# Performance work log

Measured on AMD Instinct MI355X. Metric: run time of the kernel, lower is better.

## Reference

```python
import jax, jax.numpy as jnp
import numpy as np

NEG_INIT = -1.0e9  # matches torch.full(..., -1000000000.0)

def setup_inputs() -> dict:
    key = jax.random.key(0)
    ks = jax.random.split(key, 12)
    N, B, F, C = 4_000_000, 16384, 3, 4
    flat_muons = jax.random.normal(ks[0], (N, F), dtype=jnp.float32)
    batch_index = jnp.sort(jax.random.randint(ks[1], (N,), 0, B))
    conditions = jax.random.normal(ks[2], (B, C), dtype=jnp.float32)
    def lin(k, fin, fout):
        k1, k2 = jax.random.split(k)
        bound = 1.0 / np.sqrt(fin)
        W = jax.random.uniform(k1, (fin, fout), jnp.float32, -bound, bound)
        b = jax.random.uniform(k2, (fout,), jnp.float32, -bound, bound)
        return W, b
    W1, b1 = lin(ks[3], F + C, 64)
    W2, b2 = lin(ks[4], 64, 128)
    W3, b3 = lin(ks[5], 128 + C, 128)
    W4, b4 = lin(ks[6], 128, 1)
    return {"flat_muons": flat_muons, "batch_index": batch_index,
            "conditions": conditions, "batch_size": B,
            "W1": W1, "b1": b1, "W2": W2, "b2": b2,
            "W3": W3, "b3": b3, "W4": W4, "b4": b4}

def reference(flat_muons, batch_index, conditions, batch_size,
              W1, b1, W2, b2, W3, b3, W4, b4):
    lrelu = lambda x: jax.nn.leaky_relu(x, 0.2)
    flat_cond = conditions[batch_index]                       # [N, C] gather
    point_in = jnp.concatenate([flat_muons, flat_cond], axis=1)
    h = lrelu(point_in @ W1 + b1)                             # [N, 64]
    point_feats = lrelu(h @ W2 + b2)                          # [N, 128]
    # segmented amax with -1e9 baseline (scatter_reduce_ amax semantics)
    global_feats = jnp.full((batch_size, 128), NEG_INIT, dtype=point_feats.dtype)
    global_feats = global_feats.at[batch_index].max(point_feats)
    decision_in = jnp.concatenate([global_feats, conditions], axis=1)
    score = lrelu(decision_in @ W3 + b3) @ W4 + b4            # [B, 1]
    return score
```

## Files before the change

kernel.cpp:

```cpp
#include <hip/hip_runtime.h>

typedef float f32x4 __attribute__((ext_vector_type(4)));
typedef float f32x16 __attribute__((ext_vector_type(16)));
typedef _Float16 half8 __attribute__((ext_vector_type(8)));
typedef _Float16 half2v __attribute__((ext_vector_type(2)));
typedef unsigned u32x4 __attribute__((ext_vector_type(4)));

__device__ __forceinline__ unsigned f2mono(float f) {
  unsigned u = __float_as_uint(f);
  return (u & 0x80000000u) ? ~u : (u | 0x80000000u);
}
__device__ __forceinline__ float mono2f(unsigned u) {
  return (u & 0x80000000u) ? __uint_as_float(u & 0x7fffffffu) : __uint_as_float(~u);
}
__device__ __forceinline__ float lrelu(float x) { return fmaxf(x, 0.2f * x); }
__device__ __forceinline__ unsigned pkrtz(float a, float b) {
  return __builtin_bit_cast(unsigned, __builtin_amdgcn_cvt_pkrtz(a, b));
}
__device__ __forceinline__ unsigned lrelu_pk(float a, float b) {
  const half2v v = __builtin_bit_cast(half2v, pkrtz(a, b));
  const half2v s = v * (half2v){(_Float16)0.2f, (_Float16)0.2f};
  return __builtin_bit_cast(unsigned, __builtin_elementwise_max(v, s));
}
__device__ __forceinline__ half8 ash8(u32x4 u) { return __builtin_bit_cast(half8, u); }
__device__ __forceinline__ float max16(const f32x16& a) {
  const float m1 = fmaxf(fmaxf(a[0], a[1]), a[2]);
  const float m2 = fmaxf(fmaxf(a[3], a[4]), a[5]);
  const float m3 = fmaxf(fmaxf(a[6], a[7]), a[8]);
  const float m4 = fmaxf(fmaxf(a[9], a[10]), a[11]);
  const float m5 = fmaxf(fmaxf(a[12], a[13]), a[14]);
  return fmaxf(fmaxf(fmaxf(m1, m2), m3), fmaxf(fmaxf(m4, m5), a[15]));
}
__device__ __forceinline__ void plswap(unsigned& x, unsigned& y) {
  asm volatile("v_permlane32_swap_b32 %0, %1" : "+v"(x), "+v"(y));
}
__device__ __forceinline__ float xhalf_max(float m) {
  unsigned a = __float_as_uint(m), b = a;
  plswap(a, b);
  return fmaxf(__uint_as_float(a), __uint_as_float(b));
}

__global__ void sc_init(unsigned* __restrict__ gf, int total4) {
  int i = blockIdx.x * blockDim.x + threadIdx.x;
  if (i < total4) {
    unsigned m = f2mono(-1.0e9f);
    ((uint4*)gf)[i] = make_uint4(m, m, m, m);
  }
}

__global__ __launch_bounds__(256, 2) void sc_main(
    const float* __restrict__ muons, const int* __restrict__ bidx,
    const float* __restrict__ cond, const float* __restrict__ W1,
    const float* __restrict__ b1, const float* __restrict__ W2,
    const float* __restrict__ b2, unsigned* __restrict__ gf, int N, int CPW) {
  __shared__ __align__(16) _Float16 w2f[8192];
  __shared__ __align__(16) _Float16 w1e[1024];

  const int t = threadIdx.x;
  const int w = t >> 6;
  const int lane = t & 63;
  const int col = lane & 31;
  const int kh2 = lane >> 5;

  {
    const int j = t & 127, kh = t >> 7;
    for (int kk = 0; kk < 32; ++kk) {
      const int k = kh * 32 + kk;
      w2f[((k >> 3) * 128 + j) * 8 + (k & 7)] = (_Float16)W2[k * 128 + j];
    }
  }
  if (t < 128) {
    const int j = t & 63, kc = t >> 6;
    for (int e = 0; e < 8; ++e) {
      const int kp = kc * 8 + e;
      float val;
      if (kp < 7)       val = W1[kp * 64 + j];
      else if (kp < 14) val = W1[(kp - 7) * 64 + j];
      else if (kp == 14) val = b1[j];
      else { const float b = b1[j]; val = b - (float)(_Float16)b; }
      w1e[(kc * 64 + j) * 8 + e] = (_Float16)val;
    }
  }
  __syncthreads();

  float b2v[4];
  #pragma unroll
  for (int jt = 0; jt < 4; ++jt) b2v[jt] = b2[jt * 32 + col];
  f32x16 zf;
  #pragma unroll
  for (int e = 0; e < 16; ++e) zf[e] = 0.0f;

  const int gwave = blockIdx.x * 4 + w;
  const int start = gwave * CPW;
  if (start >= N) return;
  const int end = min(start + CPW, N);
  const int prevb = (start == 0) ? -1 : bidx[start - 1];
  const int nextb = (end >= N) ? -1 : bidx[end];
  int run_b = bidx[start];
  float run_s[4];
  #pragma unroll
  for (int jt = 0; jt < 4; ++jt) run_s[jt] = -3.0e38f;

  const half8 a1lo = *(const half8*)&w1e[(kh2 * 64 + col) * 8];
  const half8 a1hi = *(const half8*)&w1e[(kh2 * 64 + 32 + col) * 8];

  auto FLUSH = [&](int b, const float* m) {
    const bool interior = (b != prevb) && (b != nextb);
    float mm[4];
    #pragma unroll
    for (int jt = 0; jt < 4; ++jt) mm[jt] = xhalf_max(m[jt]);
    if (lane < 32) {
      #pragma unroll
      for (int jt = 0; jt < 4; ++jt) {
        if (mm[jt] > -2.9e38f) {
          const unsigned enc = f2mono(lrelu(mm[jt] + b2v[jt]));
          unsigned* addr = &gf[b * 128 + jt * 32 + col];
          if (interior) *addr = enc; else atomicMax(addr, enc);
        }
      }
    }
  };

  auto DECOMP = [&](float mu0, float mu1, float mu2, const f32x4& c4) -> half8 {
    float in[7];
    in[0] = mu0; in[1] = mu1; in[2] = mu2;
    in[3] = c4.x; in[4] = c4.y; in[5] = c4.z; in[6] = c4.w;
    const unsigned pA0 = pkrtz(in[0], in[1]);
    const unsigned pA1 = pkrtz(in[2], in[3]);
    const unsigned pA2 = pkrtz(in[4], in[5]);
    const half2v hA0 = __builtin_bit_cast(half2v, pA0);
    const half2v hA1 = __builtin_bit_cast(half2v, pA1);
    const half2v hA2 = __builtin_bit_cast(half2v, pA2);
    const float xl0 = in[0] - (float)hA0[0];
    const unsigned pA3 = pkrtz(in[6], xl0);
    const half2v hA3 = __builtin_bit_cast(half2v, pA3);
    const unsigned pB0 = pkrtz(in[1] - (float)hA0[1], in[2] - (float)hA1[0]);
    const unsigned pB1 = pkrtz(in[3] - (float)hA1[1], in[4] - (float)hA2[0]);
    const unsigned pB2 = pkrtz(in[5] - (float)hA2[1], in[6] - (float)hA3[0]);
    const unsigned pB3 = 0x3C003C00u;
    u32x4 bu;
    bu[0] = kh2 ? pB0 : pA0;
    bu[1] = kh2 ? pB1 : pA1;
    bu[2] = kh2 ? pB2 : pA2;
    bu[3] = kh2 ? pB3 : pA3;
    return ash8(bu);
  };

  auto MKAFRAG = [&](const f32x16& a0, const f32x16& a1, half8* Afr) {
    unsigned pk0[8], pk1[8];
    #pragma unroll
    for (int q = 0; q < 4; ++q) {
      pk0[2 * q]     = lrelu_pk(a0[4 * q],     a0[4 * q + 1]);
      pk0[2 * q + 1] = lrelu_pk(a0[4 * q + 2], a0[4 * q + 3]);
      pk1[2 * q]     = lrelu_pk(a1[4 * q],     a1[4 * q + 1]);
      pk1[2 * q + 1] = lrelu_pk(a1[4 * q + 2], a1[4 * q + 3]);
    }
    #pragma unroll
    for (int ks = 0; ks < 4; ++ks) {
      const unsigned* s = (ks < 2) ? pk0 : pk1;
      const int base = (ks & 1) * 4;
      unsigned x0 = s[base + 0], y0 = s[base + 2];
      unsigned x1 = s[base + 1], y1 = s[base + 3];
      plswap(x0, y0);
      plswap(x1, y1);
      u32x4 au;
      au[0] = x0; au[1] = x1; au[2] = y0; au[3] = y1;
      Afr[ks] = ash8(au);
    }
  };

  auto L2SEG = [&](const half8* Afr, int bi) {
    f32x16 acc2[4];
    #pragma unroll
    for (int ks = 0; ks < 4; ++ks) {
      const int kcb = (2 * ks + kh2) * 128;
      #pragma unroll
      for (int jt = 0; jt < 4; ++jt) {
        const half8 B = *(const half8*)&w2f[(kcb + jt * 32 + col) * 8];
        acc2[jt] = __builtin_amdgcn_mfma_f32_32x32x16_f16(Afr[ks], B,
                                                          (ks == 0) ? zf : acc2[jt], 0, 0, 0);
      }
    }
    const int bA = __shfl(bi, 0);
    const int bB = __shfl(bi, 31);
    if (bA != run_b) {
      FLUSH(run_b, run_s);
      #pragma unroll
      for (int jt = 0; jt < 4; ++jt) run_s[jt] = -3.0e38f;
      run_b = bA;
    }
    if (bA == bB) {
      #pragma unroll
      for (int jt = 0; jt < 4; ++jt)
        run_s[jt] = fmaxf(run_s[jt], max16(acc2[jt]));
    } else {
      const unsigned long long ball = __ballot(bi == bA);
      const int split = (int)__popcll(ball & 0xffffffffULL);
      const int bS = __shfl(bi, split);
      if (bS == bB) {
        float mA[4], mB[4];
        #pragma unroll
        for (int jt = 0; jt < 4; ++jt) { mA[jt] = -3.0e38f; mB[jt] = -3.0e38f; }
        #pragma unroll
        for (int r = 0; r < 16; ++r) {
          const int rr = (r & 3) + ((r >> 2) << 3) + (kh2 << 2);
          const bool inA = rr < split;
          #pragma unroll
          for (int jt = 0; jt < 4; ++jt) {
            const float v = acc2[jt][r];
            mA[jt] = fmaxf(mA[jt], inA ? v : -3.0e38f);
            mB[jt] = fmaxf(mB[jt], inA ? -3.0e38f : v);
          }
        }
        #pragma unroll
        for (int jt = 0; jt < 4; ++jt) mA[jt] = fmaxf(mA[jt], run_s[jt]);
        FLUSH(bA, mA);
        #pragma unroll
        for (int jt = 0; jt < 4; ++jt) run_s[jt] = mB[jt];
        run_b = bB;
      } else {
        int pbi[16];
        #pragma unroll
        for (int r = 0; r < 16; ++r) {
          const int rr = (r & 3) + ((r >> 2) << 3) + (kh2 << 2);
          pbi[r] = __shfl(bi, rr);
        }
        for (int b = bA; b <= bB; ++b) {
          float m[4];
          #pragma unroll
          for (int jt = 0; jt < 4; ++jt) {
            float mm = -3.0e38f;
            #pragma unroll
            for (int r = 0; r < 16; ++r)
              if (pbi[r] == b) mm = fmaxf(mm, acc2[jt][r]);
            if (b == bA) mm = fmaxf(mm, run_s[jt]);
            m[jt] = mm;
          }
          if (b < bB) {
            FLUSH(b, m);
          } else {
            #pragma unroll
            for (int jt = 0; jt < 4; ++jt) run_s[jt] = m[jt];
          }
        }
        run_b = bB;
      }
    }
  };

  int pA = min(start + col, N - 1);
  int pB = min(start + 32 + col, N - 1);
  int biA_n = bidx[pA], biB_n = bidx[pB];
  float muA_n[3] = {muons[pA * 3], muons[pA * 3 + 1], muons[pA * 3 + 2]};
  float muB_n[3] = {muons[pB * 3], muons[pB * 3 + 1], muons[pB * 3 + 2]};
  f32x4 c4A_n = *(const f32x4*)&cond[biA_n * 4];
  f32x4 c4B_n = *(const f32x4*)&cond[biB_n * 4];

  for (int pbase = start; pbase < end; pbase += 64) {
    const int biA = biA_n, biB = biB_n;
    const float mA0 = muA_n[0], mA1 = muA_n[1], mA2 = muA_n[2];
    const float mB0 = muB_n[0], mB1 = muB_n[1], mB2 = muB_n[2];
    const f32x4 c4A = c4A_n, c4B = c4B_n;

    const int pnA = min(pbase + 64 + col, N - 1);
    const int pnB = min(pbase + 96 + col, N - 1);
    biA_n = bidx[pnA]; biB_n = bidx[pnB];
    muA_n[0] = muons[pnA * 3]; muA_n[1] = muons[pnA * 3 + 1]; muA_n[2] = muons[pnA * 3 + 2];
    muB_n[0] = muons[pnB * 3]; muB_n[1] = muons[pnB * 3 + 1]; muB_n[2] = muons[pnB * 3 + 2];

    const half8 bfrA = DECOMP(mA0, mA1, mA2, c4A);
    const half8 bfrB = DECOMP(mB0, mB1, mB2, c4B);
    const f32x16 aA0 = __builtin_amdgcn_mfma_f32_32x32x16_f16(a1lo, bfrA, zf, 0, 0, 0);
    const f32x16 aA1 = __builtin_amdgcn_mfma_f32_32x32x16_f16(a1hi, bfrA, zf, 0, 0, 0);
    const f32x16 aB0 = __builtin_amdgcn_mfma_f32_32x32x16_f16(a1lo, bfrB, zf, 0, 0, 0);
    const f32x16 aB1 = __builtin_amdgcn_mfma_f32_32x32x16_f16(a1hi, bfrB, zf, 0, 0, 0);

    c4A_n = *(const f32x4*)&cond[biA_n * 4];
    c4B_n = *(const f32x4*)&cond[biB_n * 4];

    half8 AfrA[4], AfrB[4];
    MKAFRAG(aA0, aA1, AfrA);
    MKAFRAG(aB0, aB1, AfrB);

    L2SEG(AfrA, biA);
    L2SEG(AfrB, biB);
  }
  FLUSH(run_b, run_s);
}

__global__ __launch_bounds__(256, 2) void sc_final(
    const unsigned* __restrict__ gf, const float* __restrict__ cond,
    const float* __restrict__ W3, const float* __restrict__ b3,
    const float* __restrict__ W4, const float* __restrict__ b4,
    float* __restrict__ out, int B) {
  __shared__ __align__(16) _Float16 w3h[18432];
  __shared__ __align__(16) _Float16 w3l[18432];
  __shared__ float w4s[128];
  const int t = threadIdx.x;
  const int w = t >> 6, lane = t & 63, col = lane & 31, kh2 = lane >> 5;

  for (int i = t; i < 144 * 128; i += 256) {
    const int k = i >> 7, j = i & 127;
    float v = 0.0f;
    if (k < 132) v = W3[k * 128 + j];
    else if (k == 132) v = b3[j];
    const _Float16 h = (_Float16)v;
    const int a = ((k >> 3) * 128 + j) * 8 + (k & 7);
    w3h[a] = h;
    w3l[a] = (_Float16)(v - (float)h);
  }
  if (t < 128) w4s[t] = W4[t];
  __syncthreads();

  const int tile = blockIdx.x * 4 + w;
  const int row = tile * 32 + col;
  const int rc = min(row, B - 1);

  uint4 g[16];
  #pragma unroll
  for (int kc = 0; kc < 8; ++kc) {
    const int base = rc * 128 + kc * 16 + kh2 * 8;
    g[2 * kc]     = *(const uint4*)&gf[base];
    g[2 * kc + 1] = *(const uint4*)&gf[base + 4];
  }
  const f32x4 c4 = *(const f32x4*)&cond[rc * 4];

  f32x16 zf;
  #pragma unroll
  for (int e = 0; e < 16; ++e) zf[e] = 0.0f;
  f32x16 acc[4];

  #pragma unroll
  for (int kc = 0; kc < 9; ++kc) {
    float v[8];
    if (kc < 8) {
      const uint4 ga = g[2 * kc], gb = g[2 * kc + 1];
      v[0] = mono2f(ga.x); v[1] = mono2f(ga.y); v[2] = mono2f(ga.z); v[3] = mono2f(ga.w);
      v[4] = mono2f(gb.x); v[5] = mono2f(gb.y); v[6] = mono2f(gb.z); v[7] = mono2f(gb.w);
    } else if (kh2 == 0) {
      v[0] = c4.x; v[1] = c4.y; v[2] = c4.z; v[3] = c4.w;
      v[4] = 1.0f; v[5] = 0.0f; v[6] = 0.0f; v[7] = 0.0f;
    } else {
      #pragma unroll
      for (int e = 0; e < 8; ++e) v[e] = 0.0f;
    }
    u32x4 bh, bl;
    #pragma unroll
    for (int q = 0; q < 4; ++q) {
      const unsigned ph = pkrtz(v[2 * q], v[2 * q + 1]);
      const half2v hh = __builtin_bit_cast(half2v, ph);
      bh[q] = ph;
      bl[q] = pkrtz(v[2 * q] - (float)hh[0], v[2 * q + 1] - (float)hh[1]);
    }
    const half8 Bh = ash8(bh), Bl = ash8(bl);
    #pragma unroll
    for (int jt = 0; jt < 4; ++jt) {
      const int a = ((kc * 2 + kh2) * 128 + jt * 32 + col) * 8;
      const half8 Ah = *(const half8*)&w3h[a];
      const half8 Al = *(const half8*)&w3l[a];
      f32x16 c = (kc == 0) ? zf : acc[jt];
      c = __builtin_amdgcn_mfma_f32_32x32x16_f16(Ah, Bh, c, 0, 0, 0);
      c = __builtin_amdgcn_mfma_f32_32x32x16_f16(Ah, Bl, c, 0, 0, 0);
      c = __builtin_amdgcn_mfma_f32_32x32x16_f16(Al, Bh, c, 0, 0, 0);
      acc[jt] = c;
    }
  }

  float partial = 0.0f;
  #pragma unroll
  for (int jt = 0; jt < 4; ++jt)
    #pragma unroll
    for (int r = 0; r < 16; ++r) {
      const int j = jt * 32 + (r & 3) + ((r >> 2) << 3) + (kh2 << 2);
      partial += lrelu(acc[jt][r]) * w4s[j];
    }
  unsigned pa = __float_as_uint(partial), pb = pa;
  plswap(pa, pb);
  const float tot = __uint_as_float(pa) + __uint_as_float(pb);
  if (lane < 32 && row < B) out[row] = tot + b4[0];
}

extern "C" void kernel_launch(void* const* d_in, const int* in_sizes, int n_in,
                              void* d_out, int out_size, void* d_ws, size_t ws_size,
                              hipStream_t stream) {
  const float* muons = (const float*)d_in[0];
  const int* bidx = (const int*)d_in[1];
  const float* cond = (const float*)d_in[2];
  const float* W1 = (const float*)d_in[4];
  const float* b1 = (const float*)d_in[5];
  const float* W2 = (const float*)d_in[6];
  const float* b2 = (const float*)d_in[7];
  const float* W3 = (const float*)d_in[8];
  const float* b3 = (const float*)d_in[9];
  const float* W4 = (const float*)d_in[10];
  const float* b4 = (const float*)d_in[11];
  float* out = (float*)d_out;
  const int N = in_sizes[1];
  const int B = out_size;
  unsigned* gf = (unsigned*)d_ws;

  const int total4 = (B * 128) / 4;
  sc_init<<<(total4 + 255) / 256, 256, 0, stream>>>(gf, total4);

  const int nblocks = 2048;
  const int nwaves = nblocks * 4;
  const int cpw = (((N + nwaves - 1) / nwaves) + 63) & ~63;
  sc_main<<<nblocks, 256, 0, stream>>>(muons, bidx, cond, W1, b1, W2, b2, gf, N, cpw);

  const int ftiles = (B + 31) / 32;
  const int fblocks = (ftiles + 3) / 4;
  sc_final<<<fblocks, 256, 0, stream>>>(gf, cond, W3, b3, W4, b4, out, B);
  (void)n_in; (void)ws_size;
}
```

Measured before the change: 124.2 us.

## Split layer-2 MFMA accumulators into halves and raise occupancy to three blocks

The layer-2 MFMA loop now computes two 32-column tiles at a time instead of all four, and the segmented max reduction and flush run per half. This cuts the number of live f32x16 accumulators from four to two, lowering register pressure. Launch bounds for sc_main go from 2 to 3 blocks per CU to use the freed registers for occupancy. The cost is that boundary-handling logic (ballot, split and shuffles) and the flush path run twice per segment, and there is less MFMA ILP within a wave.

```diff
diff --git a/kernel.cpp b/kernel.cpp
--- a/kernel.cpp
+++ b/kernel.cpp
@@ -48,7 +48,7 @@
   }
 }
 
-__global__ __launch_bounds__(256, 2) void sc_main(
+__global__ __launch_bounds__(256, 3) void sc_main(
     const float* __restrict__ muons, const int* __restrict__ bidx,
     const float* __restrict__ cond, const float* __restrict__ W1,
     const float* __restrict__ b1, const float* __restrict__ W2,
@@ -104,19 +104,20 @@
   const half8 a1lo = *(const half8*)&w1e[(kh2 * 64 + col) * 8];
   const half8 a1hi = *(const half8*)&w1e[(kh2 * 64 + 32 + col) * 8];
 
-  auto FLUSH = [&](int b, const float* m) {
+  auto FLUSH2 = [&](int b, int jtb, float m0, float m1) {
     const bool interior = (b != prevb) && (b != nextb);
-    float mm[4];
-    #pragma unroll
-    for (int jt = 0; jt < 4; ++jt) mm[jt] = xhalf_max(m[jt]);
+    const float g0 = xhalf_max(m0);
+    const float g1 = xhalf_max(m1);
     if (lane < 32) {
-      #pragma unroll
-      for (int jt = 0; jt < 4; ++jt) {
-        if (mm[jt] > -2.9e38f) {
-          const unsigned enc = f2mono(lrelu(mm[jt] + b2v[jt]));
-          unsigned* addr = &gf[b * 128 + jt * 32 + col];
-          if (interior) *addr = enc; else atomicMax(addr, enc);
-        }
+      if (g0 > -2.9e38f) {
+        const unsigned enc = f2mono(lrelu(g0 + b2v[jtb]));
+        unsigned* addr = &gf[b * 128 + jtb * 32 + col];
+        if (interior) *addr = enc; else atomicMax(addr, enc);
+      }
+      if (g1 > -2.9e38f) {
+        const unsigned enc = f2mono(lrelu(g1 + b2v[jtb + 1]));
+        unsigned* addr = &gf[b * 128 + (jtb + 1) * 32 + col];
+        if (interior) *addr = enc; else atomicMax(addr, enc);
       }
     }
   };
@@ -170,54 +171,54 @@
   };
 
   auto L2SEG = [&](const half8* Afr, int bi) {
-    f32x16 acc2[4];
-    #pragma unroll
-    for (int ks = 0; ks < 4; ++ks) {
-      const int kcb = (2 * ks + kh2) * 128;
-      #pragma unroll
-      for (int jt = 0; jt < 4; ++jt) {
-        const half8 B = *(const half8*)&w2f[(kcb + jt * 32 + col) * 8];
-        acc2[jt] = __builtin_amdgcn_mfma_f32_32x32x16_f16(Afr[ks], B,
-                                                          (ks == 0) ? zf : acc2[jt], 0, 0, 0);
-      }
-    }
     const int bA = __shfl(bi, 0);
     const int bB = __shfl(bi, 31);
     if (bA != run_b) {
-      FLUSH(run_b, run_s);
+      FLUSH2(run_b, 0, run_s[0], run_s[1]);
+      FLUSH2(run_b, 2, run_s[2], run_s[3]);
       #pragma unroll
       for (int jt = 0; jt < 4; ++jt) run_s[jt] = -3.0e38f;
       run_b = bA;
     }
-    if (bA == bB) {
+    const bool fast = (bA == bB);
+    int split = 0, bS = 0;
+    if (!fast) {
+      const unsigned long long ball = __ballot(bi == bA);
+      split = (int)__popcll(ball & 0xffffffffULL);
+      bS = __shfl(bi, split);
+    }
+
+    #pragma unroll
+    for (int jh = 0; jh < 2; ++jh) {
+      const int jt0 = jh * 2, jt1 = jh * 2 + 1;
+      f32x16 a0, a1;
       #pragma unroll
-      for (int jt = 0; jt < 4; ++jt)
-        run_s[jt] = fmaxf(run_s[jt], max16(acc2[jt]));
-    } else {
-      const unsigned long long ball = __ballot(bi == bA);
-      const int split = (int)__popcll(ball & 0xffffffffULL);
-      const int bS = __shfl(bi, split);
-      if (bS == bB) {
-        float mA[4], mB[4];
-        #pragma unroll
-        for (int jt = 0; jt < 4; ++jt) { mA[jt] = -3.0e38f; mB[jt] = -3.0e38f; }
+      for (int ks = 0; ks < 4; ++ks) {
+        const int kcb = (2 * ks + kh2) * 128;
+        const half8 B0 = *(const half8*)&w2f[(kcb + jt0 * 32 + col) * 8];
+        const half8 B1 = *(const half8*)&w2f[(kcb + jt1 * 32 + col) * 8];
+        a0 = __builtin_amdgcn_mfma_f32_32x32x16_f16(Afr[ks], B0, (ks == 0) ? zf : a0, 0, 0, 0);
+        a1 = __builtin_amdgcn_mfma_f32_32x32x16_f16(Afr[ks], B1, (ks == 0) ? zf : a1, 0, 0, 0);
+      }
+
+      if (fast) {
+        run_s[jt0] = fmaxf(run_s[jt0], max16(a0));
+        run_s[jt1] = fmaxf(run_s[jt1], max16(a1));
+      } else if (bS == bB) {
+        float mA0 = -3.0e38f, mA1 = -3.0e38f, mB0 = -3.0e38f, mB1 = -3.0e38f;
         #pragma unroll
         for (int r = 0; r < 16; ++r) {
           const int rr = (r & 3) + ((r >> 2) << 3) + (kh2 << 2);
           const bool inA = rr < split;
-          #pragma unroll
-          for (int jt = 0; jt < 4; ++jt) {
-            const float v = acc2[jt][r];
-            mA[jt] = fmaxf(mA[jt], inA ? v : -3.0e38f);
-            mB[jt] = fmaxf(mB[jt], inA ? -3.0e38f : v);
-          }
+          const float v0 = a0[r], v1 = a1[r];
+          mA0 = fmaxf(mA0, inA ? v0 : -3.0e38f);
+          mA1 = fmaxf(mA1, inA ? v1 : -3.0e38f);
+          mB0 = fmaxf(mB0, inA ? -3.0e38f : v0);
+          mB1 = fmaxf(mB1, inA ? -3.0e38f : v1);
         }
-        #pragma unroll
-        for (int jt = 0; jt < 4; ++jt) mA[jt] = fmaxf(mA[jt], run_s[jt]);
-        FLUSH(bA, mA);
-        #pragma unroll
-        for (int jt = 0; jt < 4; ++jt) run_s[jt] = mB[jt];
-        run_b = bB;
+        FLUSH2(bA, jt0, fmaxf(mA0, run_s[jt0]), fmaxf(mA1, run_s[jt1]));
+        run_s[jt0] = mB0;
+        run_s[jt1] = mB1;
       } else {
         int pbi[16];
         #pragma unroll
@@ -226,26 +227,21 @@
           pbi[r] = __shfl(bi, rr);
         }
         for (int b = bA; b <= bB; ++b) {
-          float m[4];
+          float m0 = -3.0e38f, m1 = -3.0e38f;
           #pragma unroll
-          for (int jt = 0; jt < 4; ++jt) {
-            float mm = -3.0e38f;
-            #pragma unroll
-            for (int r = 0; r < 16; ++r)
-              if (pbi[r] == b) mm = fmaxf(mm, acc2[jt][r]);
-            if (b == bA) mm = fmaxf(mm, run_s[jt]);
-            m[jt] = mm;
-          }
+          for (int r = 0; r < 16; ++r)
+            if (pbi[r] == b) { m0 = fmaxf(m0, a0[r]); m1 = fmaxf(m1, a1[r]); }
+          if (b == bA) { m0 = fmaxf(m0, run_s[jt0]); m1 = fmaxf(m1, run_s[jt1]); }
           if (b < bB) {
-            FLUSH(b, m);
+            FLUSH2(b, jt0, m0, m1);
           } else {
-            #pragma unroll
-            for (int jt = 0; jt < 4; ++jt) run_s[jt] = m[jt];
+            run_s[jt0] = m0;
+            run_s[jt1] = m1;
           }
         }
-        run_b = bB;
       }
     }
+    if (!fast) run_b = bB;
   };
 
   int pA = min(start + col, N - 1);
@@ -285,7 +281,8 @@
     L2SEG(AfrA, biA);
     L2SEG(AfrB, biB);
   }
-  FLUSH(run_b, run_s);
+  FLUSH2(run_b, 0, run_s[0], run_s[1]);
+  FLUSH2(run_b, 2, run_s[2], run_s[3]);
 }
 
 __global__ __launch_bounds__(256, 2) void sc_final(
```

After: 121.6 us. -2.1%, faster.
